# Optimization experiments

Hardware: AMD Instinct MI355X
Metric: run time of the kernel (lower is better)

## Reference

```python
import jax, jax.numpy as jnp
import numpy as np

B, N, DIM, H, DH = 4, 2048, 512, 8, 64
INNER = H * DH  # 512
SCALE = DH ** -0.5


def setup_inputs() -> dict:
    key = jax.random.key(0)
    k1, k2, k3, k4 = jax.random.split(key, 4)
    x = jax.random.normal(k1, (B, N, DIM), dtype=jnp.float32)
    bias = jax.random.normal(k2, (B, N, DIM), dtype=jnp.float32)
    # to_qkv: Linear(dim, inner*3, bias=False)
    w_qkv = jax.random.normal(k3, (DIM, 3 * INNER), dtype=jnp.float32) * (DIM ** -0.5)
    # to_out: Linear(inner, dim) with bias (project_out=True since heads != 1)
    w_out = jax.random.normal(k4, (INNER, DIM), dtype=jnp.float32) * (INNER ** -0.5)
    b_out = jnp.zeros((DIM,), dtype=jnp.float32)
    return {"x": x, "bias": bias, "w_qkv": w_qkv, "w_out": w_out, "b_out": b_out}


def _split_heads(t):
    # [b, n, h*d] -> [b, h, n, d]
    b, n, _ = t.shape
    return t.reshape(b, n, H, DH).transpose(0, 2, 1, 3)


def reference(x, bias, w_qkv, w_out, b_out):
    qkv = x @ w_qkv  # [b, n, 3*inner]
    q, k, v = jnp.split(qkv, 3, axis=-1)
    q, k, v = map(_split_heads, (q, k, v))
    dots = jnp.einsum('bhid,bhjd->bhij', q, k) * SCALE  # [b,h,n,n]

    qkv_b = bias @ w_qkv
    qb, kb, _ = jnp.split(qkv_b, 3, axis=-1)
    qb, kb = _split_heads(qb), _split_heads(kb)
    dots = dots + jnp.einsum('bhid,bhjd->bhij', qb, kb) * SCALE

    attn = jax.nn.softmax(dots, axis=-1)
    out = jnp.einsum('bhij,bhjd->bhid', attn, v)  # [b,h,n,d]
    out = out.transpose(0, 2, 1, 3).reshape(x.shape[0], x.shape[1], INNER)
    return out @ w_out + b_out
```

## Files before the change

### kernel.cpp

```cpp
#include <hip/hip_runtime.h>
#include <hip/hip_bf16.h>

#define DEV __device__ __forceinline__

typedef __attribute__((ext_vector_type(8))) short short8;
typedef __attribute__((ext_vector_type(4))) int i32x4;
typedef __attribute__((ext_vector_type(2))) int i32x2;
typedef __attribute__((ext_vector_type(4))) float f32x4;
typedef __attribute__((ext_vector_type(16))) float f32x16;

constexpr int B = 4, N = 2048, H = 8, DH = 64;
constexpr int INNER = H * DH;
constexpr int BH = B * H;
constexpr float QSCALE = 0.125f * 1.44269504088896f;

constexpr size_t OFF_WQKVT = 0;
constexpr size_t OFF_WOUTT = OFF_WQKVT + (size_t)1536 * 512;
constexpr size_t OFF_QT    = OFF_WOUTT + (size_t)512 * 512;
constexpr size_t OFF_KT    = OFF_QT + (size_t)BH * N * 128;
constexpr size_t OFF_VT    = OFF_KT + (size_t)BH * N * 128;
constexpr size_t OFF_AO    = OFF_VT + (size_t)BH * DH * N;
constexpr size_t OFF_XBF   = OFF_AO + (size_t)8192 * 512;
constexpr size_t OFF_BBF   = OFF_AO;

DEV short f2b(float f) {
    __hip_bfloat16 h = __float2bfloat16(f);
    return __builtin_bit_cast(short, h);
}

DEV int cvtpk(float lo, float hi) {
    int r;
    asm("v_cvt_pk_bf16_f32 %0, %1, %2" : "=v"(r) : "v"(lo), "v"(hi));
    return r;
}

DEV float fexp2(float x) {
    float r;
    asm("v_exp_f32 %0, %1" : "=v"(r) : "v"(x));
    return r;
}

DEV void plswap(int& a, int& b) {
    i32x2 r = __builtin_amdgcn_permlane32_swap(a, b, false, false);
    a = r.x; b = r.y;
}

DEV void gload16(const void* g, void* l) {
    __builtin_amdgcn_global_load_lds(
        (const __attribute__((address_space(1))) unsigned int*)g,
        (__attribute__((address_space(3))) unsigned int*)l, 16, 0, 0);
}

__global__ void prep_kernel(const float* __restrict__ wqkv,
                            const float* __restrict__ wout,
                            const float* __restrict__ x,
                            const float* __restrict__ bias,
                            __hip_bfloat16* __restrict__ ws) {
    __hip_bfloat16* wqkvT = ws + OFF_WQKVT;
    __hip_bfloat16* woutT = ws + OFF_WOUTT;
    short8* xbf = (short8*)(ws + OFF_XBF);
    short8* bbf = (short8*)(ws + OFF_BBF);
    int tid = blockIdx.x * blockDim.x + threadIdx.x;
    const int nconv = 8192 * 512 / 8;
    const int t1 = 512 * 1536 / 4;
    const int t2 = 512 * 512 / 4;
    const int total = 2 * nconv + t1 + t2;
    for (int i = tid; i < total; i += gridDim.x * blockDim.x) {
        if (i < 2 * nconv) {
            const float4* src = (const float4*)(i < nconv ? x : bias);
            short8* dst = i < nconv ? xbf : bbf;
            int j = i < nconv ? i : i - nconv;
            float4 v0 = src[2 * j], v1 = src[2 * j + 1];
            short8 sv;
            sv[0] = f2b(v0.x); sv[1] = f2b(v0.y); sv[2] = f2b(v0.z); sv[3] = f2b(v0.w);
            sv[4] = f2b(v1.x); sv[5] = f2b(v1.y); sv[6] = f2b(v1.z); sv[7] = f2b(v1.w);
            dst[j] = sv;
        } else if (i < 2 * nconv + t1) {
            int j = i - 2 * nconv;
            int k  = j / 384;
            int c4 = (j % 384) * 4;
            float4 v = ((const float4*)wqkv)[j];
            wqkvT[(size_t)(c4 + 0) * 512 + k] = __float2bfloat16(v.x);
            wqkvT[(size_t)(c4 + 1) * 512 + k] = __float2bfloat16(v.y);
            wqkvT[(size_t)(c4 + 2) * 512 + k] = __float2bfloat16(v.z);
            wqkvT[(size_t)(c4 + 3) * 512 + k] = __float2bfloat16(v.w);
        } else {
            int j = i - 2 * nconv - t1;
            int k  = j / 128;
            int c4 = (j % 128) * 4;
            float4 v = ((const float4*)wout)[j];
            woutT[(size_t)(c4 + 0) * 512 + k] = __float2bfloat16(v.x);
            woutT[(size_t)(c4 + 1) * 512 + k] = __float2bfloat16(v.y);
            woutT[(size_t)(c4 + 2) * 512 + k] = __float2bfloat16(v.z);
            woutT[(size_t)(c4 + 3) * 512 + k] = __float2bfloat16(v.w);
        }
    }
}

__global__ __launch_bounds__(256) void gemm_qkv(__hip_bfloat16* __restrict__ ws) {
    int mt = blockIdx.x, yt = blockIdx.y;
    bool src_is_bias = (yt >= 12);
    int nt = src_is_bias ? yt - 12 : yt;
    const short* A  = (const short*)(ws + (src_is_bias ? OFF_BBF : OFF_XBF));
    const short* Bt = (const short*)(ws + OFF_WQKVT);
    int m0 = mt * 128, n0 = nt * 128;

    __shared__ __align__(16) short As[128][64];
    __shared__ __align__(16) short Bs[128][64];

    int tid  = threadIdx.x;
    int wave = tid >> 6, lane = tid & 63;
    int wrow = wave >> 1, wcol = wave & 1;
    int lg = lane >> 4, li = lane & 15;

    f32x4 acc[4][4] = {};

    for (int k0 = 0; k0 < 512; k0 += 64) {
#pragma unroll
        for (int i = 0; i < 4; ++i) {
            int c = wave * 4 + i;
            int r = c * 8 + (lane >> 3);
            gload16((const char*)A + ((size_t)(m0 + r) * 512 + k0 + (lane & 7) * 8) * 2,
                    (char*)&As[0][0] + c * 1024);
            gload16((const char*)Bt + ((size_t)(n0 + r) * 512 + k0 + (lane & 7) * 8) * 2,
                    (char*)&Bs[0][0] + c * 1024);
        }
        __syncthreads();
#pragma unroll
        for (int ks = 0; ks < 2; ++ks) {
            short8 af[4], bf[4];
#pragma unroll
            for (int m = 0; m < 4; ++m)
                af[m] = *(const short8*)(&As[wrow * 64 + m * 16 + li][ks * 32 + lg * 8]);
#pragma unroll
            for (int n = 0; n < 4; ++n)
                bf[n] = *(const short8*)(&Bs[wcol * 64 + n * 16 + li][ks * 32 + lg * 8]);
#pragma unroll
            for (int m = 0; m < 4; ++m)
#pragma unroll
                for (int n = 0; n < 4; ++n)
                    acc[m][n] = __builtin_amdgcn_mfma_f32_16x16x32_bf16(af[m], bf[n], acc[m][n], 0, 0, 0);
        }
        __syncthreads();
    }

    __hip_bfloat16* QT = ws + OFF_QT;
    __hip_bfloat16* KT = ws + OFF_KT;
    __hip_bfloat16* VT = ws + OFF_VT;
    int qkoff = src_is_bias ? 64 : 0;
#pragma unroll
    for (int m = 0; m < 4; ++m)
#pragma unroll
        for (int n = 0; n < 4; ++n)
#pragma unroll
            for (int j = 0; j < 4; ++j) {
                int row = m0 + wrow * 64 + m * 16 + lg * 4 + j;
                int col = n0 + wcol * 64 + n * 16 + li;
                float v = acc[m][n][j];
                int b = row >> 11, nn = row & 2047;
                if (col < 512) {
                    int h = col >> 6, d = col & 63;
                    QT[((size_t)(b * H + h) * N + nn) * 128 + d + qkoff] = __float2bfloat16(v * QSCALE);
                } else if (col < 1024) {
                    int c = col - 512; int h = c >> 6, d = c & 63;
                    KT[((size_t)(b * H + h) * N + nn) * 128 + d + qkoff] = __float2bfloat16(v);
                } else {
                    int c = col - 1024; int h = c >> 6, d = c & 63;
                    VT[((size_t)(b * H + h) * DH + d) * N + nn] = __float2bfloat16(v);
                }
            }
}

__global__ __launch_bounds__(256, 3) void attn_kernel(__hip_bfloat16* __restrict__ ws) {
    int bid = blockIdx.x;
    int c   = bid & 7;
    int idx = bid >> 3;
    int bh  = (idx & 3) * 8 + c;
    int qb  = idx >> 2;

    int wave = threadIdx.x >> 6, lane = threadIdx.x & 63;
    int li32 = lane & 31, hi = lane >> 5;
    int qr0 = qb * 128 + wave * 32;

    const short* QT  = (const short*)(ws + OFF_QT) + (size_t)bh * N * 128;
    const char*  KTg = (const char*)((const short*)(ws + OFF_KT) + (size_t)bh * N * 128);
    const char*  VTg = (const char*)((const short*)(ws + OFF_VT) + (size_t)bh * DH * N);

    __shared__ __align__(16) short Ktile[2][64][128];
    __shared__ __align__(16) short Vtile[2][64][64];

    short8 qf[8];
#pragma unroll
    for (int kc = 0; kc < 8; ++kc)
        qf[kc] = *(const short8*)(QT + (size_t)(qr0 + li32) * 128 + kc * 16 + hi * 8);

    float m_run = -3e38f, l_run = 0.f;
    f32x16 o[2] = {};

    auto stage = [&](int t, int b) {
        int kv0 = t * 64;
#pragma unroll
        for (int cc = 0; cc < 4; ++cc) {
            int ck = wave * 4 + cc;
            int r  = ck * 4 + (lane >> 4);
            int cbx = (lane & 15) * 16;
            gload16(KTg + (size_t)(kv0 + r) * 256 + (cbx ^ ((r & 7) << 4)),
                    (char*)&Ktile[b][0][0] + ck * 1024);
        }
#pragma unroll
        for (int cc = 0; cc < 2; ++cc) {
            int ck = wave * 2 + cc;
            int r  = ck * 8 + (lane >> 3);
            int cbx = (lane & 7) * 16;
            gload16(VTg + (size_t)r * 4096 + kv0 * 2 + (cbx ^ ((r & 7) << 4)),
                    (char*)&Vtile[b][0][0] + ck * 1024);
        }
    };

    stage(0, 0);
    __syncthreads();
    int buf = 0;

    for (int t = 0; t < N / 64; ++t) {
        if (t + 1 < N / 64) stage(t + 1, buf ^ 1);
        const char* Kb = (const char*)&Ktile[buf][0][0];
        const char* Vb = (const char*)&Vtile[buf][0][0];

        f32x16 sT[2] = {};
        __builtin_amdgcn_s_setprio(1);
#pragma unroll
        for (int sub = 0; sub < 2; ++sub) {
            int row = sub * 32 + li32;
            int sw  = (row & 7) << 4;
            const char* kbase = Kb + row * 256;
#pragma unroll
            for (int kc = 0; kc < 8; ++kc) {
                short8 kf = *(const short8*)(kbase + ((kc * 32 + hi * 16) ^ sw));
                sT[sub] = __builtin_amdgcn_mfma_f32_32x32x16_bf16(kf, qf[kc], sT[sub], 0, 0, 0);
            }
        }
        __builtin_amdgcn_s_setprio(0);

        float t0[8];
#pragma unroll
        for (int j = 0; j < 8; ++j)
            t0[j] = fmaxf(fmaxf(sT[0][j], sT[0][j + 8]), fmaxf(sT[1][j], sT[1][j + 8]));
        float pm = fmaxf(fmaxf(fmaxf(t0[0], t0[1]), fmaxf(t0[2], t0[3])),
                         fmaxf(fmaxf(t0[4], t0[5]), fmaxf(t0[6], t0[7])));
        pm = fmaxf(pm, __shfl_xor(pm, 32));

        if (__any(pm > m_run + 8.f)) {
            float mn = fmaxf(m_run, pm);
            float al = fexp2(m_run - mn);
#pragma unroll
            for (int a = 0; a < 2; ++a)
#pragma unroll
                for (int r = 0; r < 16; ++r) o[a][r] *= al;
            l_run *= al;
            m_run = mn;
        }

        float lsp[4] = {0.f, 0.f, 0.f, 0.f};
        int w[2][8];
#pragma unroll
        for (int sub = 0; sub < 2; ++sub)
#pragma unroll
            for (int r2 = 0; r2 < 8; ++r2) {
                float p0 = fexp2(sT[sub][2 * r2]     - m_run);
                float p1 = fexp2(sT[sub][2 * r2 + 1] - m_run);
                lsp[r2 & 3] += p0 + p1;
                w[sub][r2] = cvtpk(p0, p1);
            }
        l_run += (lsp[0] + lsp[1]) + (lsp[2] + lsp[3]);

        short8 pf[2][2];
#pragma unroll
        for (int sub = 0; sub < 2; ++sub) {
            plswap(w[sub][0], w[sub][2]); plswap(w[sub][1], w[sub][3]);
            plswap(w[sub][4], w[sub][6]); plswap(w[sub][5], w[sub][7]);
            i32x4 f0 = { w[sub][0], w[sub][1], w[sub][2], w[sub][3] };
            i32x4 f1 = { w[sub][4], w[sub][5], w[sub][6], w[sub][7] };
            pf[sub][0] = __builtin_bit_cast(short8, f0);
            pf[sub][1] = __builtin_bit_cast(short8, f1);
        }

        __builtin_amdgcn_s_setprio(1);
#pragma unroll
        for (int sub = 0; sub < 2; ++sub)
#pragma unroll
            for (int ksel = 0; ksel < 2; ++ksel) {
                int cc = sub * 2 + ksel;
#pragma unroll
                for (int a = 0; a < 2; ++a) {
                    int row = a * 32 + li32;
                    int sw  = (row & 7) << 4;
                    short8 vf = *(const short8*)(Vb + row * 128 + ((cc * 32 + hi * 16) ^ sw));
                    o[a] = __builtin_amdgcn_mfma_f32_32x32x16_bf16(vf, pf[sub][ksel], o[a], 0, 0, 0);
                }
            }
        __builtin_amdgcn_s_setprio(0);

        __syncthreads();
        buf ^= 1;
    }

    l_run += __shfl_xor(l_run, 32);
    __hip_bfloat16* AO = ws + OFF_AO;
    int b = bh >> 3, h = bh & 7;
    char* tb = (char*)&Ktile[0][0][0] + wave * 4096;
    float inv = 1.f / l_run;
#pragma unroll
    for (int a = 0; a < 2; ++a)
#pragma unroll
        for (int r2 = 0; r2 < 8; ++r2) {
            int r = 2 * r2;
            int dv = (r & 3) + 8 * (r >> 2) + 4 * hi + 32 * a;
            int word = cvtpk(o[a][r] * inv, o[a][r + 1] * inv);
            *(int*)(tb + li32 * 128 + ((dv * 2) ^ ((li32 & 7) << 4))) = word;
        }
#pragma unroll
    for (int qq = 0; qq < 32; qq += 8) {
        int q = qq + (lane >> 3), seg = lane & 7;
        short8 vrow = *(const short8*)(tb + q * 128 + ((seg * 16) ^ ((q & 7) << 4)));
        *(short8*)(AO + (size_t)(b * N + qr0 + q) * INNER + h * 64 + seg * 8) = vrow;
    }
}

__global__ __launch_bounds__(256) void gemm_out(const __hip_bfloat16* __restrict__ ws_c,
                                                const float* __restrict__ bout,
                                                float* __restrict__ out) {
    const short* AO = (const short*)(ws_c + OFF_AO);
    const short* Bt = (const short*)(ws_c + OFF_WOUTT);
    int m0 = blockIdx.x * 128, n0 = blockIdx.y * 128;

    __shared__ __align__(16) short As[128][64];
    __shared__ __align__(16) short Bs[128][64];

    int tid  = threadIdx.x;
    int wave = tid >> 6, lane = tid & 63;
    int wrow = wave >> 1, wcol = wave & 1;
    int lg = lane >> 4, li = lane & 15;

    f32x4 acc[4][4] = {};

    for (int k0 = 0; k0 < 512; k0 += 64) {
#pragma unroll
        for (int i = 0; i < 4; ++i) {
            int c = wave * 4 + i;
            int r = c * 8 + (lane >> 3);
            gload16((const char*)AO + ((size_t)(m0 + r) * 512 + k0 + (lane & 7) * 8) * 2,
                    (char*)&As[0][0] + c * 1024);
            gload16((const char*)Bt + ((size_t)(n0 + r) * 512 + k0 + (lane & 7) * 8) * 2,
                    (char*)&Bs[0][0] + c * 1024);
        }
        __syncthreads();
#pragma unroll
        for (int ks = 0; ks < 2; ++ks) {
            short8 af[4], bf[4];
#pragma unroll
            for (int m = 0; m < 4; ++m)
                af[m] = *(const short8*)(&As[wrow * 64 + m * 16 + li][ks * 32 + lg * 8]);
#pragma unroll
            for (int n = 0; n < 4; ++n)
                bf[n] = *(const short8*)(&Bs[wcol * 64 + n * 16 + li][ks * 32 + lg * 8]);
#pragma unroll
            for (int m = 0; m < 4; ++m)
#pragma unroll
                for (int n = 0; n < 4; ++n)
                    acc[m][n] = __builtin_amdgcn_mfma_f32_16x16x32_bf16(af[m], bf[n], acc[m][n], 0, 0, 0);
        }
        __syncthreads();
    }
#pragma unroll
    for (int m = 0; m < 4; ++m)
#pragma unroll
        for (int n = 0; n < 4; ++n)
#pragma unroll
            for (int j = 0; j < 4; ++j) {
                int row = m0 + wrow * 64 + m * 16 + lg * 4 + j;
                int col = n0 + wcol * 64 + n * 16 + li;
                out[(size_t)row * 512 + col] = acc[m][n][j] + bout[col];
            }
}

extern "C" void kernel_launch(void* const* d_in, const int* in_sizes, int n_in,
                              void* d_out, int out_size, void* d_ws, size_t ws_size,
                              hipStream_t stream) {
    const float* x    = (const float*)d_in[0];
    const float* bias = (const float*)d_in[1];
    const float* wqkv = (const float*)d_in[2];
    const float* wout = (const float*)d_in[3];
    const float* bout = (const float*)d_in[4];
    float* out = (float*)d_out;
    __hip_bfloat16* ws = (__hip_bfloat16*)d_ws;

    hipLaunchKernelGGL(prep_kernel, dim3(2048), dim3(256), 0, stream, wqkv, wout, x, bias, ws);
    hipLaunchKernelGGL(gemm_qkv, dim3(64, 20), dim3(256), 0, stream, ws);
    hipLaunchKernelGGL(attn_kernel, dim3(512), dim3(256), 0, stream, ws);
    hipLaunchKernelGGL(gemm_out, dim3(64, 4), dim3(256), 0, stream, (const __hip_bfloat16*)ws, bout, out);
}
```

Baseline: 144.8 us.

## Vectorize GEMM epilogue stores via MFMA operand swap and unroll attention double-buffer

The QKV and output GEMMs swap the MFMA A/B operands so that each lane holds four consecutive output columns. The epilogue can then write packed bf16 pairs (8-byte stores) or float4s instead of scattered scalar stores. For the transposed V output the original operand order is kept, which gives contiguous sequence positions and packed stores there too. The attention loop is unrolled by two with constant buffer pointers, removing the dynamic buffer index; this adds code size and branching in the GEMM.

```diff
diff --git a/kernel.cpp b/kernel.cpp
--- a/kernel.cpp
+++ b/kernel.cpp
@@ -104,6 +104,7 @@
     const short* A  = (const short*)(ws + (src_is_bias ? OFF_BBF : OFF_XBF));
     const short* Bt = (const short*)(ws + OFF_WQKVT);
     int m0 = mt * 128, n0 = nt * 128;
+    bool isV = (!src_is_bias && nt >= 8);
 
     __shared__ __align__(16) short As[128][64];
     __shared__ __align__(16) short Bs[128][64];
@@ -115,60 +116,90 @@
 
     f32x4 acc[4][4] = {};
 
-    for (int k0 = 0; k0 < 512; k0 += 64) {
-#pragma unroll
-        for (int i = 0; i < 4; ++i) {
-            int c = wave * 4 + i;
-            int r = c * 8 + (lane >> 3);
-            gload16((const char*)A + ((size_t)(m0 + r) * 512 + k0 + (lane & 7) * 8) * 2,
-                    (char*)&As[0][0] + c * 1024);
-            gload16((const char*)Bt + ((size_t)(n0 + r) * 512 + k0 + (lane & 7) * 8) * 2,
-                    (char*)&Bs[0][0] + c * 1024);
-        }
-        __syncthreads();
-#pragma unroll
-        for (int ks = 0; ks < 2; ++ks) {
-            short8 af[4], bf[4];
-#pragma unroll
-            for (int m = 0; m < 4; ++m)
-                af[m] = *(const short8*)(&As[wrow * 64 + m * 16 + li][ks * 32 + lg * 8]);
-#pragma unroll
-            for (int n = 0; n < 4; ++n)
-                bf[n] = *(const short8*)(&Bs[wcol * 64 + n * 16 + li][ks * 32 + lg * 8]);
-#pragma unroll
-            for (int m = 0; m < 4; ++m)
+    auto kloop = [&](bool swp) {
+        for (int k0 = 0; k0 < 512; k0 += 64) {
+#pragma unroll
+            for (int i = 0; i < 4; ++i) {
+                int c = wave * 4 + i;
+                int r = c * 8 + (lane >> 3);
+                gload16((const char*)A + ((size_t)(m0 + r) * 512 + k0 + (lane & 7) * 8) * 2,
+                        (char*)&As[0][0] + c * 1024);
+                gload16((const char*)Bt + ((size_t)(n0 + r) * 512 + k0 + (lane & 7) * 8) * 2,
+                        (char*)&Bs[0][0] + c * 1024);
+            }
+            __syncthreads();
+#pragma unroll
+            for (int ks = 0; ks < 2; ++ks) {
+                short8 af[4], bf[4];
+#pragma unroll
+                for (int m = 0; m < 4; ++m)
+                    af[m] = *(const short8*)(&As[wrow * 64 + m * 16 + li][ks * 32 + lg * 8]);
 #pragma unroll
                 for (int n = 0; n < 4; ++n)
-                    acc[m][n] = __builtin_amdgcn_mfma_f32_16x16x32_bf16(af[m], bf[n], acc[m][n], 0, 0, 0);
-        }
-        __syncthreads();
-    }
+                    bf[n] = *(const short8*)(&Bs[wcol * 64 + n * 16 + li][ks * 32 + lg * 8]);
+#pragma unroll
+                for (int m = 0; m < 4; ++m)
+#pragma unroll
+                    for (int n = 0; n < 4; ++n)
+                        acc[m][n] = swp
+                            ? __builtin_amdgcn_mfma_f32_16x16x32_bf16(bf[n], af[m], acc[m][n], 0, 0, 0)
+                            : __builtin_amdgcn_mfma_f32_16x16x32_bf16(af[m], bf[n], acc[m][n], 0, 0, 0);
+            }
+            __syncthreads();
+        }
+    };
+    if (isV) kloop(false); else kloop(true);
 
     __hip_bfloat16* QT = ws + OFF_QT;
     __hip_bfloat16* KT = ws + OFF_KT;
     __hip_bfloat16* VT = ws + OFF_VT;
-    int qkoff = src_is_bias ? 64 : 0;
-#pragma unroll
-    for (int m = 0; m < 4; ++m)
-#pragma unroll
-        for (int n = 0; n < 4; ++n)
-#pragma unroll
-            for (int j = 0; j < 4; ++j) {
-                int row = m0 + wrow * 64 + m * 16 + lg * 4 + j;
-                int col = n0 + wcol * 64 + n * 16 + li;
-                float v = acc[m][n][j];
-                int b = row >> 11, nn = row & 2047;
-                if (col < 512) {
-                    int h = col >> 6, d = col & 63;
-                    QT[((size_t)(b * H + h) * N + nn) * 128 + d + qkoff] = __float2bfloat16(v * QSCALE);
-                } else if (col < 1024) {
-                    int c = col - 512; int h = c >> 6, d = c & 63;
-                    KT[((size_t)(b * H + h) * N + nn) * 128 + d + qkoff] = __float2bfloat16(v);
+
+    if (isV) {
+        int cc_base = n0 - 1024 + wcol * 64;
+#pragma unroll
+        for (int m = 0; m < 4; ++m) {
+            int row0 = m0 + wrow * 64 + m * 16 + lg * 4;
+            int b = row0 >> 11, nn = row0 & 2047;
+#pragma unroll
+            for (int n = 0; n < 4; ++n) {
+                int cc = cc_base + n * 16 + li;
+                int h = cc >> 6, d = cc & 63;
+                int w0 = cvtpk(acc[m][n][0], acc[m][n][1]);
+                int w1 = cvtpk(acc[m][n][2], acc[m][n][3]);
+                short* p = (short*)VT + (size_t)((b * H + h) * DH + d) * N + nn;
+                i32x2 wv = { w0, w1 };
+                *(i32x2*)p = wv;
+            }
+        }
+    } else {
+        int qkoff = src_is_bias ? 64 : 0;
+        bool isQ = (n0 < 512);
+#pragma unroll
+        for (int m = 0; m < 4; ++m) {
+            int row = m0 + wrow * 64 + m * 16 + li;
+            int b = row >> 11, nn = row & 2047;
+#pragma unroll
+            for (int n = 0; n < 4; ++n) {
+                int cc0 = n0 + wcol * 64 + n * 16 + lg * 4;
+                int w0, w1;
+                short* p;
+                if (isQ) {
+                    int h = cc0 >> 6, d0 = (cc0 & 63) + qkoff;
+                    w0 = cvtpk(acc[m][n][0] * QSCALE, acc[m][n][1] * QSCALE);
+                    w1 = cvtpk(acc[m][n][2] * QSCALE, acc[m][n][3] * QSCALE);
+                    p = (short*)QT + ((size_t)(b * H + h) * N + nn) * 128 + d0;
                 } else {
-                    int c = col - 1024; int h = c >> 6, d = c & 63;
-                    VT[((size_t)(b * H + h) * DH + d) * N + nn] = __float2bfloat16(v);
+                    int c = cc0 - 512;
+                    int h = c >> 6, d0 = (c & 63) + qkoff;
+                    w0 = cvtpk(acc[m][n][0], acc[m][n][1]);
+                    w1 = cvtpk(acc[m][n][2], acc[m][n][3]);
+                    p = (short*)KT + ((size_t)(b * H + h) * N + nn) * 128 + d0;
                 }
-            }
+                i32x2 wv = { w0, w1 };
+                *(i32x2*)p = wv;
+            }
+        }
+    }
 }
 
 __global__ __launch_bounds__(256, 3) void attn_kernel(__hip_bfloat16* __restrict__ ws) {
@@ -217,15 +248,12 @@
         }
     };
 
-    stage(0, 0);
-    __syncthreads();
-    int buf = 0;
-
-    for (int t = 0; t < N / 64; ++t) {
-        if (t + 1 < N / 64) stage(t + 1, buf ^ 1);
-        const char* Kb = (const char*)&Ktile[buf][0][0];
-        const char* Vb = (const char*)&Vtile[buf][0][0];
-
+    const char* Kb0 = (const char*)&Ktile[0][0][0];
+    const char* Kb1 = (const char*)&Ktile[1][0][0];
+    const char* Vb0 = (const char*)&Vtile[0][0][0];
+    const char* Vb1 = (const char*)&Vtile[1][0][0];
+
+    auto tile = [&](const char* Kb, const char* Vb) {
         f32x16 sT[2] = {};
         __builtin_amdgcn_s_setprio(1);
 #pragma unroll
@@ -301,7 +329,16 @@
         __builtin_amdgcn_s_setprio(0);
 
         __syncthreads();
-        buf ^= 1;
+    };
+
+    stage(0, 0);
+    __syncthreads();
+
+    for (int t = 0; t < 32; t += 2) {
+        stage(t + 1, 1);
+        tile(Kb0, Vb0);
+        if (t + 2 < 32) stage(t + 2, 0);
+        tile(Kb1, Vb1);
     }
 
     l_run += __shfl_xor(l_run, 32);
@@ -367,20 +404,26 @@
             for (int m = 0; m < 4; ++m)
 #pragma unroll
                 for (int n = 0; n < 4; ++n)
-                    acc[m][n] = __builtin_amdgcn_mfma_f32_16x16x32_bf16(af[m], bf[n], acc[m][n], 0, 0, 0);
+                    acc[m][n] = __builtin_amdgcn_mfma_f32_16x16x32_bf16(bf[n], af[m], acc[m][n], 0, 0, 0);
         }
         __syncthreads();
     }
-#pragma unroll
-    for (int m = 0; m < 4; ++m)
-#pragma unroll
-        for (int n = 0; n < 4; ++n)
-#pragma unroll
-            for (int j = 0; j < 4; ++j) {
-                int row = m0 + wrow * 64 + m * 16 + lg * 4 + j;
-                int col = n0 + wcol * 64 + n * 16 + li;
-                out[(size_t)row * 512 + col] = acc[m][n][j] + bout[col];
-            }
+
+    float4 bb[4];
+#pragma unroll
+    for (int n = 0; n < 4; ++n)
+        bb[n] = *(const float4*)(bout + n0 + wcol * 64 + n * 16 + lg * 4);
+#pragma unroll
+    for (int m = 0; m < 4; ++m) {
+        int row = m0 + wrow * 64 + m * 16 + li;
+#pragma unroll
+        for (int n = 0; n < 4; ++n) {
+            int c0 = n0 + wcol * 64 + n * 16 + lg * 4;
+            float4 v = { acc[m][n][0] + bb[n].x, acc[m][n][1] + bb[n].y,
+                         acc[m][n][2] + bb[n].z, acc[m][n][3] + bb[n].w };
+            *(float4*)(out + (size_t)row * 512 + c0) = v;
+        }
+    }
 }
 
 extern "C" void kernel_launch(void* const* d_in, const int* in_sizes, int n_in,
```

Measured after the change: 139.1 us, median of 3. 3.9% less time.
